# Kernel optimization log

Measured on AMD Instinct MI355X. Metric: run time of the kernel, lower is better.

The kernel has to match this reference:

```python
import jax, jax.numpy as jnp
import numpy as np

H = 4
C = 140
N0, E0 = 20000, 320000
N1, E1 = 5000, 80000
N2, E2 = 20000 // 16, 20000
N2, E2 = 1250, 20000
NSAME = 10  # conv02,11,12,21,22,14,15,16,04,05 (all 140->140)


def _seg_mean(v, idx, n):
    s = jax.ops.segment_sum(v, idx, num_segments=n)
    cnt = jax.ops.segment_sum(jnp.ones((idx.shape[0],), v.dtype), idx, num_segments=n)
    return s / jnp.maximum(cnt, 1.0)[:, None]


def _feast_conv(x, ei, W, u, c, b, n):
    # PyG FeaStConv, mean aggregation, no self loops.
    src, dst = ei[0], ei[1]
    xj = x[src]               # (E, Cin) neighbor (source) features
    xi = x[dst]               # (E, Cin) center (target) features
    q = jax.nn.softmax((xj - xi) @ u + c, axis=-1)            # (E, H)
    m = (xj @ W).reshape(xj.shape[0], H, -1)                  # (E, H, Cout)
    msg = jnp.einsum('eh,ehc->ec', q, m)                      # (E, Cout)
    return _seg_mean(msg, dst, n) + b


def _ln(h, g, be):
    mu = h.mean(-1, keepdims=True)
    v = ((h - mu) ** 2).mean(-1, keepdims=True)
    return (h - mu) * jax.lax.rsqrt(v + 1e-5) * g + be


def _block(x, ei, n, W, u, c, b, g=None, be=None, sW=None, sb=None, relu=True):
    h = _feast_conv(x, ei, W, u, c, b, n)
    if g is not None:
        h = _ln(h, g, be)
    skip = x if sW is None else x @ sW + sb
    h = h + skip
    if relu:
        h = jax.nn.relu(h)
    return h


def setup_inputs() -> dict:
    key = jax.random.key(0)
    ks = iter(jax.random.split(key, 80))

    def nrm(shape, s=0.05):
        return jax.random.normal(next(ks), shape, jnp.float32) * s

    inp = {}
    inp['x'] = jax.random.normal(next(ks), (N0, 4), jnp.float32)
    inp['e0'] = jax.random.randint(next(ks), (2, E0), 0, N0)
    inp['e1'] = jax.random.randint(next(ks), (2, E1), 0, N1)
    inp['e2'] = jax.random.randint(next(ks), (2, E2), 0, N2)
    inp['cl1'] = jax.random.randint(next(ks), (N0,), 0, N1)
    inp['cl2'] = jax.random.randint(next(ks), (N1,), 0, N2)
    inp['n0'], inp['n1'], inp['n2'] = N0, N1, N2
    # conv01: 4 -> 140 (linear skip)
    inp['W01'] = nrm((4, H * C)); inp['u01'] = nrm((4, H)); inp['c01'] = nrm((H,))
    inp['b01'] = nrm((C,)); inp['sW01'] = nrm((4, C)); inp['sb01'] = nrm((C,))
    inp['g01'] = jnp.ones((C,)); inp['be01'] = jnp.zeros((C,))
    # 10 stacked 140->140 blocks (identity skip)
    inp['Ws'] = nrm((NSAME, C, H * C)); inp['us'] = nrm((NSAME, C, H))
    inp['cs'] = nrm((NSAME, H)); inp['bs'] = nrm((NSAME, C))
    inp['gs'] = jnp.ones((NSAME, C)); inp['bes'] = jnp.zeros((NSAME, C))
    # 2 concat blocks: 280 -> 140 (conv13, conv03), linear skip
    inp['Wc'] = nrm((2, 2 * C, H * C)); inp['uc'] = nrm((2, 2 * C, H))
    inp['cc'] = nrm((2, H)); inp['bc'] = nrm((2, C))
    inp['sWc'] = nrm((2, 2 * C, C)); inp['sbc'] = nrm((2, C))
    inp['gc'] = jnp.ones((2, C)); inp['bec'] = jnp.zeros((2, C))
    # conv06: 140 -> 1, no LN, no relu, linear skip
    inp['Wo'] = nrm((C, H * 1)); inp['uo'] = nrm((C, H)); inp['co'] = nrm((H,))
    inp['bo'] = nrm((1,)); inp['sWo'] = nrm((C, 1)); inp['sbo'] = nrm((1,))
    return inp


def reference(x, W01, u01, c01, b01, sW01, sb01, g01, be01,
              Ws, us, cs, bs, gs, bes,
              Wc, uc, cc, bc, sWc, sbc, gc, bec,
              Wo, uo, co, bo, sWo, sbo,
              e0, e1, e2, cl1, cl2, n0, n1, n2):
    def same(h, i, ei, n):
        return _block(h, ei, n, Ws[i], us[i], cs[i], bs[i], gs[i], bes[i])

    def catblk(h, i, ei, n):
        return _block(h, ei, n, Wc[i], uc[i], cc[i], bc[i], gc[i], bec[i], sWc[i], sbc[i])

    h = _block(x, e0, n0, W01, u01, c01, b01, g01, be01, sW01, sb01)  # conv01
    h = same(h, 0, e0, n0)                                            # conv02
    copy0 = h
    h1 = _seg_mean(h, cl1, n1)                                        # pool1
    h1 = same(h1, 1, e1, n1)                                          # conv11
    h1 = same(h1, 2, e1, n1)                                          # conv12
    copy1 = h1
    h2 = _seg_mean(h1, cl2, n2)                                       # pool2
    h2 = same(h2, 3, e2, n2)                                          # conv21
    h2 = same(h2, 4, e2, n2)                                          # conv22
    h1 = h2[cl2]                                                      # unpool2
    h1 = jnp.concatenate((h1, copy1), axis=1)
    h1 = catblk(h1, 0, e1, n1)                                        # conv13
    h1 = same(h1, 5, e1, n1)                                          # conv14
    h1 = same(h1, 6, e1, n1)                                          # conv15
    h1 = same(h1, 7, e1, n1)                                          # conv16
    h = h1[cl1]                                                       # unpool1
    h = jnp.concatenate((h, copy0), axis=1)
    h = catblk(h, 1, e0, n0)                                          # conv03
    h = same(h, 8, e0, n0)                                            # conv04
    h = same(h, 9, e0, n0)                                            # conv05
    h = _block(h, e0, n0, Wo, uo, co, bo, None, None, sWo, sbo, relu=False)  # conv06
    return h.reshape(-1, 1)
```

## Files before the change

### kernel.cpp

```cpp
#include <hip/hip_runtime.h>
#include <math.h>

#define HH 4
#define CC 140
#define HALF 160

typedef __attribute__((ext_vector_type(8))) short short8;
typedef __attribute__((ext_vector_type(8))) _Float16 half8;
typedef __attribute__((ext_vector_type(4))) float f32x4;
typedef __attribute__((ext_vector_type(2))) _Float16 h2;
typedef unsigned short u16;

__device__ inline u16 f2h(float x) {
  union { _Float16 h; u16 u; } v; v.h = (_Float16)x; return v.u;
}
__device__ inline float h2f(u16 u) {
  union { _Float16 h; u16 u; } v; v.u = u; return (float)v.h;
}
__device__ inline h2 u2h2(unsigned u) {
  union { unsigned u; h2 h; } v; v.u = u; return v.h;
}
__device__ inline float dot2(h2 a, h2 b, float c) {
#if __has_builtin(__builtin_amdgcn_fdot2)
  return __builtin_amdgcn_fdot2(a, b, c, false);
#else
  return c + (float)a[0] * (float)b[0] + (float)a[1] * (float)b[1];
#endif
}

__global__ __launch_bounds__(256) void k_zero_i32(int* __restrict__ p, int n) {
  int i = blockIdx.x * 256 + threadIdx.x;
  if (i < n) p[i] = 0;
}
__global__ __launch_bounds__(256) void k_hist_all(
    const int* __restrict__ e0, int nE0, const int* __restrict__ e1, int nE1,
    const int* __restrict__ e2, int nE2, const int* __restrict__ cl1, int n0,
    const int* __restrict__ cl2, int n1,
    int* __restrict__ c0, int* __restrict__ c1, int* __restrict__ c2,
    int* __restrict__ c3, int* __restrict__ c4) {
  int j = blockIdx.x * 256 + threadIdx.x;
  if (j < nE0) { atomicAdd(&c0[e0[nE0 + j]], 1); return; }
  j -= nE0;
  if (j < nE1) { atomicAdd(&c1[e1[nE1 + j]], 1); return; }
  j -= nE1;
  if (j < nE2) { atomicAdd(&c2[e2[nE2 + j]], 1); return; }
  j -= nE2;
  if (j < n0) { atomicAdd(&c3[cl1[j]], 1); return; }
  j -= n0;
  if (j < n1) { atomicAdd(&c4[cl2[j]], 1); }
}
__global__ __launch_bounds__(1024) void k_exscan5(
    int* __restrict__ c0, int n0, int* __restrict__ r0,
    int* __restrict__ c1, int n1, int* __restrict__ r1,
    int* __restrict__ c2, int n2, int* __restrict__ r2,
    int* __restrict__ c3, int n3, int* __restrict__ r3,
    int* __restrict__ c4, int n4, int* __restrict__ r4) {
  int* in; int n; int* out;
  switch (blockIdx.x) {
    case 0: in = c0; n = n0; out = r0; break;
    case 1: in = c1; n = n1; out = r1; break;
    case 2: in = c2; n = n2; out = r2; break;
    case 3: in = c3; n = n3; out = r3; break;
    default: in = c4; n = n4; out = r4; break;
  }
  __shared__ int buf[1024];
  __shared__ int carry_s;
  if (threadIdx.x == 0) carry_s = 0;
  __syncthreads();
  for (int base = 0; base < n; base += 1024) {
    int i = base + (int)threadIdx.x;
    int v = (i < n) ? in[i] : 0;
    buf[threadIdx.x] = v;
    __syncthreads();
    int x = v;
    for (int off = 1; off < 1024; off <<= 1) {
      int t = (threadIdx.x >= (unsigned)off) ? buf[threadIdx.x - off] : 0;
      __syncthreads();
      x += t;
      buf[threadIdx.x] = x;
      __syncthreads();
    }
    int carry = carry_s;
    if (i < n) {
      int pref = carry + x - v;
      out[i] = pref;
      in[i] = pref;
    }
    __syncthreads();
    if (threadIdx.x == 1023) carry_s = carry + buf[1023];
    __syncthreads();
  }
  if (threadIdx.x == 0) out[n] = carry_s;
}
__global__ __launch_bounds__(256) void k_scatter_all(
    const int* __restrict__ e0, int nE0, const int* __restrict__ e1, int nE1,
    const int* __restrict__ e2, int nE2, const int* __restrict__ cl1, int n0,
    const int* __restrict__ cl2, int n1,
    int* __restrict__ c0, int* __restrict__ c1, int* __restrict__ c2,
    int* __restrict__ c3, int* __restrict__ c4,
    int* __restrict__ s0, int* __restrict__ s1, int* __restrict__ s2,
    int* __restrict__ s3, int* __restrict__ s4) {
  int j = blockIdx.x * 256 + threadIdx.x;
  if (j < nE0) { int p = atomicAdd(&c0[e0[nE0 + j]], 1); s0[p] = e0[j]; return; }
  j -= nE0;
  if (j < nE1) { int p = atomicAdd(&c1[e1[nE1 + j]], 1); s1[p] = e1[j]; return; }
  j -= nE1;
  if (j < nE2) { int p = atomicAdd(&c2[e2[nE2 + j]], 1); s2[p] = e2[j]; return; }
  j -= nE2;
  if (j < n0) { int p = atomicAdd(&c3[cl1[j]], 1); s3[p] = j; return; }
  j -= n0;
  if (j < n1) { int p = atomicAdd(&c4[cl2[j]], 1); s4[p] = j; }
}

__device__ inline void pack_one(int idx, const float* __restrict__ W,
                                const float* __restrict__ u, const float* __restrict__ sW,
                                u16* __restrict__ out, int C, int K1, int K2, int Kpad) {
  int col = idx / Kpad, kp = idx - col * Kpad;
  int ksrc = -1;
  if (kp < K1) ksrc = kp;
  else if (kp >= HALF && kp - HALF < K2) ksrc = K1 + (kp - HALF);
  float v = 0.f;
  if (ksrc >= 0) {
    if (col < 4 * C) {
      int c = col >> 2, h = col & 3;
      v = W[(size_t)ksrc * 4 * C + h * C + c];
    } else if (col < 4 * C + 4) {
      v = u[(size_t)ksrc * 4 + (col - 4 * C)];
    } else if (sW && col < 5 * C + 4) {
      v = sW[(size_t)ksrc * C + (col - 4 * C - 4)];
    }
  }
  out[idx] = f2h(v);
}
#define P01 (704 * 32)
#define PCAT (704 * 320)
#define PO (64 * 160)
#define PS (576 * 160)
__global__ __launch_bounds__(256) void k_pack_all(
    const float* __restrict__ W01, const float* __restrict__ u01, const float* __restrict__ sW01,
    const float* __restrict__ Wc, const float* __restrict__ uc, const float* __restrict__ sWc,
    const float* __restrict__ Wo, const float* __restrict__ uo, const float* __restrict__ sWo,
    const float* __restrict__ Ws, const float* __restrict__ us,
    const float* __restrict__ x,
    u16* __restrict__ Bp01, u16* __restrict__ Bpc0, u16* __restrict__ Bpc1,
    u16* __restrict__ Bpo, u16* __restrict__ Bps_all, u16* __restrict__ xb, int N0) {
  int j = blockIdx.x * 256 + threadIdx.x;
  if (j < P01) { pack_one(j, W01, u01, sW01, Bp01, CC, 4, 0, 32); return; }
  j -= P01;
  if (j < PCAT) { pack_one(j, Wc, uc, sWc, Bpc0, CC, CC, CC, 320); return; }
  j -= PCAT;
  if (j < PCAT) {
    pack_one(j, Wc + (size_t)2 * CC * HH * CC, uc + (size_t)2 * CC * HH,
             sWc + (size_t)2 * CC * CC, Bpc1, CC, CC, CC, 320);
    return;
  }
  j -= PCAT;
  if (j < PO) { pack_one(j, Wo, uo, sWo, Bpo, 1, CC, 0, 160); return; }
  j -= PO;
  if (j < 10 * PS) {
    int layer = j / PS, r = j - layer * PS;
    pack_one(r, Ws + (size_t)layer * CC * 4 * CC, us + (size_t)layer * CC * 4, nullptr,
             Bps_all + (size_t)layer * PS, CC, CC, 0, 160);
    return;
  }
  j -= 10 * PS;
  if (j < N0 * 32) {
    int i = j >> 5, c = j & 31;
    xb[j] = f2h(c < 4 ? x[(size_t)i * 4 + c] : 0.f);
  }
}

__global__ __launch_bounds__(256) void k_gemm_mfma(
    const u16* __restrict__ A1, const u16* __restrict__ A2,
    const int* __restrict__ amap, const u16* __restrict__ Bp,
    u16* __restrict__ Gy, float* __restrict__ Gl, float* __restrict__ Gs,
    int yEnd, int Cs, int N, int Kpad, int lda1) {
  __shared__ __align__(16) u16 As[128 * 32];
  __shared__ __align__(16) u16 Bs[64 * 32];
  const int tid = threadIdx.x;
  const int row0 = blockIdx.y * 128, col0 = blockIdx.x * 64;
  const int w = tid >> 6, lane = tid & 63;
  const int wm = w >> 1, wn = w & 1;
  const int arow = lane & 15, chunk = lane >> 4;
  const int swz = chunk ^ (arow & 3);
  f32x4 acc[4][2];
#pragma unroll
  for (int i = 0; i < 4; ++i)
#pragma unroll
    for (int j = 0; j < 2; ++j) acc[i][j] = (f32x4){0.f, 0.f, 0.f, 0.f};
  const int sar = tid >> 1;
  const int sak = (tid & 1) * 16;
  const int sbc = tid >> 2;
  const int sbk = (tid & 3) * 8;
  for (int k0 = 0; k0 < Kpad; k0 += 32) {
    {
      int gr = row0 + sar;
      short8 v0 = {0, 0, 0, 0, 0, 0, 0, 0}, v1 = v0;
      if (gr < N) {
        int kp0 = k0 + sak;
        const u16* b_;
        int rr, kk, ld;
        if (A2 && kp0 >= HALF) {
          b_ = A2; rr = gr; kk = kp0 - HALF; ld = HALF;
        } else {
          b_ = A1; rr = amap ? amap[gr] : gr; kk = kp0; ld = lda1;
        }
        const u16* p = b_ + (size_t)rr * ld + kk;
        v0 = *(const short8*)(p);
        v1 = *(const short8*)(p + 8);
      }
      int c0 = sak >> 3, sw = sar & 3;
      *(short8*)(As + sar * 32 + ((c0 ^ sw) << 3)) = v0;
      *(short8*)(As + sar * 32 + (((c0 + 1) ^ sw) << 3)) = v1;
    }
    {
      int gc = col0 + sbc;
      short8 v = *(const short8*)(Bp + (size_t)gc * Kpad + k0 + sbk);
      int c = sbk >> 3, sw = sbc & 3;
      *(short8*)(Bs + sbc * 32 + ((c ^ sw) << 3)) = v;
    }
    __syncthreads();
    half8 bf[2], af[4];
#pragma unroll
    for (int ni = 0; ni < 2; ++ni) {
      int col = wn * 32 + ni * 16 + arow;
      bf[ni] = *(const half8*)(Bs + col * 32 + (swz << 3));
    }
#pragma unroll
    for (int mi = 0; mi < 4; ++mi) {
      int r = wm * 64 + mi * 16 + arow;
      af[mi] = *(const half8*)(As + r * 32 + (swz << 3));
    }
#pragma unroll
    for (int mi = 0; mi < 4; ++mi)
#pragma unroll
      for (int ni = 0; ni < 2; ++ni)
        acc[mi][ni] = __builtin_amdgcn_mfma_f32_16x16x32_f16(af[mi], bf[ni], acc[mi][ni], 0, 0, 0);
    __syncthreads();
  }
  const int crow = (lane >> 4) * 4, ccol = lane & 15;
#pragma unroll
  for (int mi = 0; mi < 4; ++mi) {
    int gr0 = row0 + wm * 64 + mi * 16 + crow;
#pragma unroll
    for (int ni = 0; ni < 2; ++ni) {
      int gc = col0 + wn * 32 + ni * 16 + ccol;
#pragma unroll
      for (int j = 0; j < 4; ++j) {
        int gr = gr0 + j;
        if (gr >= N) continue;
        float v = acc[mi][ni][j];
        if (gc < yEnd) Gy[(size_t)gr * yEnd + gc] = f2h(v);
        else if (gc < yEnd + 4) Gl[(size_t)gr * 4 + (gc - yEnd)] = v;
        else if (gc < yEnd + 4 + Cs) Gs[(size_t)gr * Cs + (gc - yEnd - 4)] = v;
      }
    }
  }
}

__global__ __launch_bounds__(256) void k_agg(
    const u16* __restrict__ Gy, const float* __restrict__ Gl,
    const float* __restrict__ cv, const float* __restrict__ bias,
    const float* __restrict__ g, const float* __restrict__ be,
    const u16* __restrict__ skipA,
    const float* __restrict__ Gs, const float* __restrict__ sb,
    const int* __restrict__ rp, const int* __restrict__ sl,
    u16* __restrict__ outA, int n, int relu) {
  int wid = blockIdx.x * 4 + ((int)threadIdx.x >> 6);
  int lane = threadIdx.x & 63;
  if (wid >= n) return;
  float4 la = *(const float4*)(Gl + (size_t)wid * 4);
  float d0 = cv[0] - la.x, d1 = cv[1] - la.y;
  float d2 = cv[2] - la.z, d3 = cv[3] - la.w;
  int eb = rp[wid], ee = rp[wid + 1];
  const int c0 = lane, c1 = lane + 64, c2 = lane + 128;
  const bool h2v = c2 < CC;
  float acc0 = 0.f, acc1 = 0.f, acc2 = 0.f;
  for (int base = eb; base < ee; base += 64) {
    int m = min(ee - base, 64);
    int sreg = 0;
    int q01 = 0, q23 = 0;
    if (lane < m) {
      sreg = sl[base + lane];
      float4 lg = *(const float4*)(Gl + (size_t)sreg * 4);
      float t0 = lg.x + d0, t1 = lg.y + d1, t2 = lg.z + d2, t3 = lg.w + d3;
      float mx = fmaxf(fmaxf(t0, t1), fmaxf(t2, t3));
      float q0 = __expf(t0 - mx), q1 = __expf(t1 - mx);
      float q2 = __expf(t2 - mx), q3 = __expf(t3 - mx);
      float qi = 1.f / (q0 + q1 + q2 + q3);
      q01 = (int)((unsigned)f2h(q0 * qi) | ((unsigned)f2h(q1 * qi) << 16));
      q23 = (int)((unsigned)f2h(q2 * qi) | ((unsigned)f2h(q3 * qi) << 16));
    }
    for (int jb = 0; jb < m; jb += 8) {
      uint2 Y0[8], Y1[8], Y2[8];
      unsigned P01v[8], P23v[8];
#pragma unroll
      for (int t = 0; t < 8; ++t) {
        int j = jb + t;
        int s = __shfl(sreg, j);
        unsigned p01 = (unsigned)__shfl(q01, j);
        unsigned p23 = (unsigned)__shfl(q23, j);
        bool v = (j < m);
        P01v[t] = v ? p01 : 0u;
        P23v[t] = v ? p23 : 0u;
        if (v) {
          const u16* gy = Gy + (size_t)s * 560;
          Y0[t] = *(const uint2*)(gy + (c0 << 2));
          Y1[t] = *(const uint2*)(gy + (c1 << 2));
          Y2[t] = h2v ? *(const uint2*)(gy + (c2 << 2)) : make_uint2(0u, 0u);
        } else {
          Y0[t] = make_uint2(0u, 0u);
          Y1[t] = make_uint2(0u, 0u);
          Y2[t] = make_uint2(0u, 0u);
        }
      }
#pragma unroll
      for (int t = 0; t < 8; ++t) {
        h2 p01 = u2h2(P01v[t]), p23 = u2h2(P23v[t]);
        acc0 = dot2(u2h2(Y0[t].x), p01, acc0);
        acc0 = dot2(u2h2(Y0[t].y), p23, acc0);
        acc1 = dot2(u2h2(Y1[t].x), p01, acc1);
        acc1 = dot2(u2h2(Y1[t].y), p23, acc1);
        acc2 = dot2(u2h2(Y2[t].x), p01, acc2);
        acc2 = dot2(u2h2(Y2[t].y), p23, acc2);
      }
    }
  }
  int cnt = ee - eb;
  float inv = 1.f / (float)(cnt > 1 ? cnt : 1);
  float v0 = acc0 * inv + bias[c0];
  float v1 = acc1 * inv + bias[c1];
  float v2 = h2v ? acc2 * inv + bias[c2] : 0.f;
  if (g) {
    float s1 = v0 + v1 + v2;
    float s2 = v0 * v0 + v1 * v1 + v2 * v2;
#pragma unroll
    for (int off = 32; off > 0; off >>= 1) {
      s1 += __shfl_xor(s1, off);
      s2 += __shfl_xor(s2, off);
    }
    float mu = s1 * (1.0f / CC);
    float var = s2 * (1.0f / CC) - mu * mu;
    float r = rsqrtf(var + 1e-5f);
    v0 = (v0 - mu) * r * g[c0] + be[c0];
    v1 = (v1 - mu) * r * g[c1] + be[c1];
    if (h2v) v2 = (v2 - mu) * r * g[c2] + be[c2];
  }
  if (skipA) {
    const u16* sk = skipA + (size_t)wid * HALF;
    v0 += h2f(sk[c0]);
    v1 += h2f(sk[c1]);
    if (h2v) v2 += h2f(sk[c2]);
  } else {
    const float* gsr = Gs + (size_t)wid * CC;
    v0 += gsr[c0] + sb[c0];
    v1 += gsr[c1] + sb[c1];
    if (h2v) v2 += gsr[c2] + sb[c2];
  }
  if (relu) {
    v0 = fmaxf(v0, 0.f); v1 = fmaxf(v1, 0.f); v2 = fmaxf(v2, 0.f);
  }
  u16* oa = outA + (size_t)wid * HALF;
  oa[c0] = f2h(v0);
  oa[c1] = f2h(v1);
  if (h2v) oa[c2] = f2h(v2);
  else if (c2 < HALF) oa[c2] = 0;
}

__global__ __launch_bounds__(256) void k_out(
    const u16* __restrict__ Gy, const float* __restrict__ Gl,
    const float* __restrict__ cv, const float* __restrict__ bo,
    const float* __restrict__ Gs, const float* __restrict__ sbo,
    const int* __restrict__ rp, const int* __restrict__ sl,
    float* __restrict__ out, int n) {
  int wid = blockIdx.x * 4 + ((int)threadIdx.x >> 6);
  int lane = threadIdx.x & 63;
  if (wid >= n) return;
  float4 la = *(const float4*)(Gl + (size_t)wid * 4);
  float d0 = cv[0] - la.x, d1 = cv[1] - la.y;
  float d2 = cv[2] - la.z, d3 = cv[3] - la.w;
  int eb = rp[wid], ee = rp[wid + 1];
  float part = 0.f;
  for (int e = eb + lane; e < ee; e += 64) {
    int s = sl[e];
    float4 lg = *(const float4*)(Gl + (size_t)s * 4);
    float t0 = lg.x + d0, t1 = lg.y + d1, t2 = lg.z + d2, t3 = lg.w + d3;
    float m = fmaxf(fmaxf(t0, t1), fmaxf(t2, t3));
    float q0 = __expf(t0 - m), q1 = __expf(t1 - m), q2 = __expf(t2 - m), q3 = __expf(t3 - m);
    float qi = 1.f / (q0 + q1 + q2 + q3);
    uint2 y = *(const uint2*)(Gy + (size_t)s * 4);
    h2 y01 = u2h2(y.x), y23 = u2h2(y.y);
    part += (q0 * (float)y01[0] + q1 * (float)y01[1] +
             q2 * (float)y23[0] + q3 * (float)y23[1]) * qi;
  }
#pragma unroll
  for (int off = 32; off > 0; off >>= 1) part += __shfl_xor(part, off);
  if (lane == 0) {
    int cnt = ee - eb;
    out[wid] = part / (float)(cnt > 1 ? cnt : 1) + bo[0] + Gs[wid] + sbo[0];
  }
}

__global__ __launch_bounds__(256) void k_pool(const u16* __restrict__ inA,
                                              const int* __restrict__ rp,
                                              const int* __restrict__ sl,
                                              u16* __restrict__ outA, int nseg) {
  int wid = blockIdx.x * 4 + ((int)threadIdx.x >> 6);
  int lane = threadIdx.x & 63;
  if (wid >= nseg) return;
  int a = rp[wid], b = rp[wid + 1];
  const int c0 = lane, c1 = lane + 64, c2 = lane + 128;
  const bool h2v = c2 < CC;
  float acc0 = 0.f, acc1 = 0.f, acc2 = 0.f;
  for (int s = a; s < b; ++s) {
    size_t off = (size_t)sl[s] * HALF;
    acc0 += h2f(inA[off + c0]);
    acc1 += h2f(inA[off + c1]);
    if (h2v) acc2 += h2f(inA[off + c2]);
  }
  int cnt = b - a;
  float inv = 1.f / (float)(cnt > 1 ? cnt : 1);
  u16* oa = outA + (size_t)wid * HALF;
  oa[c0] = f2h(acc0 * inv);
  oa[c1] = f2h(acc1 * inv);
  if (h2v) oa[c2] = f2h(acc2 * inv);
  else if (c2 < HALF) oa[c2] = 0;
}

extern "C" void kernel_launch(void* const* d_in, const int* in_sizes, int n_in,
                              void* d_out, int out_size, void* d_ws, size_t ws_size,
                              hipStream_t stream) {
  (void)n_in; (void)out_size;
  const float* x    = (const float*)d_in[0];
  const int*   e0   = (const int*)d_in[1];
  const int*   e1   = (const int*)d_in[2];
  const int*   e2   = (const int*)d_in[3];
  const int*   cl1  = (const int*)d_in[4];
  const int*   cl2  = (const int*)d_in[5];
  const float* W01  = (const float*)d_in[9];
  const float* u01  = (const float*)d_in[10];
  const float* c01  = (const float*)d_in[11];
  const float* b01  = (const float*)d_in[12];
  const float* sW01 = (const float*)d_in[13];
  const float* sb01 = (const float*)d_in[14];
  const float* g01  = (const float*)d_in[15];
  const float* be01 = (const float*)d_in[16];
  const float* Ws   = (const float*)d_in[17];
  const float* us   = (const float*)d_in[18];
  const float* cs   = (const float*)d_in[19];
  const float* bs   = (const float*)d_in[20];
  const float* gs   = (const float*)d_in[21];
  const float* bes  = (const float*)d_in[22];
  const float* Wc   = (const float*)d_in[23];
  const float* uc   = (const float*)d_in[24];
  const float* cc   = (const float*)d_in[25];
  const float* bc   = (const float*)d_in[26];
  const float* sWc  = (const float*)d_in[27];
  const float* sbc  = (const float*)d_in[28];
  const float* gc   = (const float*)d_in[29];
  const float* bec  = (const float*)d_in[30];
  const float* Wo   = (const float*)d_in[31];
  const float* uo   = (const float*)d_in[32];
  const float* co   = (const float*)d_in[33];
  const float* bo   = (const float*)d_in[34];
  const float* sWo  = (const float*)d_in[35];
  const float* sbo  = (const float*)d_in[36];

  const int N0 = in_sizes[0] / 4;
  const int nE0 = in_sizes[1] / 2;
  const int nE1 = in_sizes[2] / 2;
  const int nE2 = in_sizes[3] / 2;
  const int N1 = 5000, N2 = 1250;

  float* fp = (float*)d_ws;
  auto alloc_f = [&](size_t n) { n = (n + 15) & ~(size_t)15; float* p = fp; fp += n; return p; };
  auto alloc_h = [&](size_t n) { return (u16*)alloc_f((n + 1) / 2); };
  u16*   Gy = alloc_h((size_t)N0 * 560);
  float* Gl = alloc_f((size_t)N0 * 4);
  float* Gs = alloc_f((size_t)N0 * CC);
  u16* a0A = alloc_h((size_t)N0 * HALF);
  u16* a0B = alloc_h((size_t)N0 * HALF);
  u16* a1A = alloc_h((size_t)N1 * HALF);
  u16* a1B = alloc_h((size_t)N1 * HALF);
  u16* a2A = alloc_h((size_t)N2 * HALF);
  u16* a2B = alloc_h((size_t)N2 * HALF);
  u16* xb  = alloc_h((size_t)N0 * 32);
  u16* Bp01 = alloc_h(P01);
  u16* Bpc0 = alloc_h(PCAT);
  u16* Bpc1 = alloc_h(PCAT);
  u16* Bpo  = alloc_h(PO);
  u16* Bps_all = alloc_h((size_t)10 * PS);
  u16* Bps[10];
  for (int i = 0; i < 10; ++i) Bps[i] = Bps_all + (size_t)i * PS;
  int* ipb = (int*)fp;
  auto alloc_i = [&](size_t n) { int* p = ipb; ipb += n; return p; };
  int* rp0  = alloc_i(N0 + 1);
  int* sl0  = alloc_i(nE0);
  int* rp1  = alloc_i(N1 + 1);
  int* sl1  = alloc_i(nE1);
  int* rp2  = alloc_i(N2 + 1);
  int* sl2  = alloc_i(nE2);
  int* rpc1 = alloc_i(N1 + 1);
  int* slc1 = alloc_i(N0);
  int* rpc2 = alloc_i(N2 + 1);
  int* slc2 = alloc_i(N1);
  int* cur0 = alloc_i(N0);
  int* cur1 = alloc_i(N1);
  int* cur2 = alloc_i(N2);
  int* cur3 = alloc_i(N1);
  int* cur4 = alloc_i(N2);
  const int curTot = N0 + N1 + N2 + N1 + N2;
  if ((size_t)((char*)ipb - (char*)d_ws) > ws_size) return;

  auto cdiv = [](int a, int b) { return (a + b - 1) / b; };

  k_zero_i32<<<cdiv(curTot, 256), 256, 0, stream>>>(cur0, curTot);
  {
    int tot = nE0 + nE1 + nE2 + N0 + N1;
    k_hist_all<<<cdiv(tot, 256), 256, 0, stream>>>(e0, nE0, e1, nE1, e2, nE2, cl1, N0, cl2, N1,
                                                   cur0, cur1, cur2, cur3, cur4);
    k_exscan5<<<5, 1024, 0, stream>>>(cur0, N0, rp0, cur1, N1, rp1, cur2, N2, rp2,
                                      cur3, N1, rpc1, cur4, N2, rpc2);
    k_scatter_all<<<cdiv(tot, 256), 256, 0, stream>>>(e0, nE0, e1, nE1, e2, nE2, cl1, N0, cl2, N1,
                                                      cur0, cur1, cur2, cur3, cur4,
                                                      sl0, sl1, sl2, slc1, slc2);
  }
  {
    int tot = P01 + 2 * PCAT + PO + 10 * PS + N0 * 32;
    k_pack_all<<<cdiv(tot, 256), 256, 0, stream>>>(W01, u01, sW01, Wc, uc, sWc, Wo, uo, sWo,
                                                   Ws, us, x, Bp01, Bpc0, Bpc1, Bpo,
                                                   Bps_all, xb, N0);
  }

  auto do_conv = [&](const u16* A1, const u16* A2, const int* amap, int Kpad, int lda1,
                     const u16* Bp, int Mld, bool hasSkip, int n, const int* rp, const int* sl,
                     const float* cp, const float* bp, const float* gp, const float* bep,
                     const u16* skipA, const float* sbp, u16* outA) {
    dim3 grid(Mld / 64, cdiv(n, 128));
    k_gemm_mfma<<<grid, 256, 0, stream>>>(A1, A2, amap, Bp, Gy, Gl, Gs,
                                          560, hasSkip ? CC : 0, n, Kpad, lda1);
    k_agg<<<cdiv(n, 4), 256, 0, stream>>>(Gy, Gl, cp, bp, gp, bep, skipA, Gs, sbp,
                                          rp, sl, outA, n, 1);
  };

  auto ci  = [&](int i) { return cs + (size_t)i * HH; };
  auto bi  = [&](int i) { return bs + (size_t)i * CC; };
  auto gi  = [&](int i) { return gs + (size_t)i * CC; };
  auto bei = [&](int i) { return bes + (size_t)i * CC; };

  do_conv(xb, nullptr, nullptr, 32, 32, Bp01, 704, true, N0, rp0, sl0,
          c01, b01, g01, be01, nullptr, sb01, a0A);
  do_conv(a0A, nullptr, nullptr, 160, HALF, Bps[0], 576, false, N0, rp0, sl0,
          ci(0), bi(0), gi(0), bei(0), a0A, nullptr, a0B);
  k_pool<<<cdiv(N1, 4), 256, 0, stream>>>(a0B, rpc1, slc1, a1A, N1);
  do_conv(a1A, nullptr, nullptr, 160, HALF, Bps[1], 576, false, N1, rp1, sl1,
          ci(1), bi(1), gi(1), bei(1), a1A, nullptr, a1B);
  do_conv(a1B, nullptr, nullptr, 160, HALF, Bps[2], 576, false, N1, rp1, sl1,
          ci(2), bi(2), gi(2), bei(2), a1B, nullptr, a1A);
  k_pool<<<cdiv(N2, 4), 256, 0, stream>>>(a1A, rpc2, slc2, a2A, N2);
  do_conv(a2A, nullptr, nullptr, 160, HALF, Bps[3], 576, false, N2, rp2, sl2,
          ci(3), bi(3), gi(3), bei(3), a2A, nullptr, a2B);
  do_conv(a2B, nullptr, nullptr, 160, HALF, Bps[4], 576, false, N2, rp2, sl2,
          ci(4), bi(4), gi(4), bei(4), a2B, nullptr, a2A);
  do_conv(a2A, a1A, cl2, 320, HALF, Bpc0, 704, true, N1, rp1, sl1,
          cc, bc, gc, bec, nullptr, sbc, a1B);
  do_conv(a1B, nullptr, nullptr, 160, HALF, Bps[5], 576, false, N1, rp1, sl1,
          ci(5), bi(5), gi(5), bei(5), a1B, nullptr, a1A);
  do_conv(a1A, nullptr, nullptr, 160, HALF, Bps[6], 576, false, N1, rp1, sl1,
          ci(6), bi(6), gi(6), bei(6), a1A, nullptr, a1B);
  do_conv(a1B, nullptr, nullptr, 160, HALF, Bps[7], 576, false, N1, rp1, sl1,
          ci(7), bi(7), gi(7), bei(7), a1B, nullptr, a1A);
  do_conv(a1A, a0B, cl1, 320, HALF, Bpc1, 704, true, N0, rp0, sl0,
          cc + HH, bc + CC, gc + CC, bec + CC, nullptr, sbc + CC, a0A);
  do_conv(a0A, nullptr, nullptr, 160, HALF, Bps[8], 576, false, N0, rp0, sl0,
          ci(8), bi(8), gi(8), bei(8), a0A, nullptr, a0B);
  do_conv(a0B, nullptr, nullptr, 160, HALF, Bps[9], 576, false, N0, rp0, sl0,
          ci(9), bi(9), gi(9), bei(9), a0B, nullptr, a0A);
  {
    dim3 grid(1, cdiv(N0, 128));
    k_gemm_mfma<<<grid, 256, 0, stream>>>(a0A, nullptr, nullptr, Bpo, Gy, Gl, Gs,
                                          4, 1, N0, 160, HALF);
    k_out<<<cdiv(N0, 4), 256, 0, stream>>>(Gy, Gl, co, bo, Gs, sbo, rp0, sl0, (float*)d_out, N0);
  }
}
```

Measured before the change: 670.3 us.

## Load MFMA operands directly from global memory, dropping LDS staging and barriers

The MFMA GEMM no longer stages A and B tiles through shared memory. Each lane now loads its half8 fragments straight from global memory using row pointers precomputed once per block, and the two __syncthreads per K step are gone. This removes LDS write/read traffic and barrier stalls. In exchange, tiles are reloaded redundantly across waves (wn pairs share A, wm pairs share B) and the loads become less coalesced. Out-of-range rows are clamped to N-1 instead of zero-filled, which is safe because those rows are never stored.

```diff
diff --git a/kernel.cpp b/kernel.cpp
--- a/kernel.cpp
+++ b/kernel.cpp
@@ -175,68 +175,52 @@
     const int* __restrict__ amap, const u16* __restrict__ Bp,
     u16* __restrict__ Gy, float* __restrict__ Gl, float* __restrict__ Gs,
     int yEnd, int Cs, int N, int Kpad, int lda1) {
-  __shared__ __align__(16) u16 As[128 * 32];
-  __shared__ __align__(16) u16 Bs[64 * 32];
   const int tid = threadIdx.x;
   const int row0 = blockIdx.y * 128, col0 = blockIdx.x * 64;
   const int w = tid >> 6, lane = tid & 63;
   const int wm = w >> 1, wn = w & 1;
   const int arow = lane & 15, chunk = lane >> 4;
-  const int swz = chunk ^ (arow & 3);
   f32x4 acc[4][2];
 #pragma unroll
   for (int i = 0; i < 4; ++i)
 #pragma unroll
     for (int j = 0; j < 2; ++j) acc[i][j] = (f32x4){0.f, 0.f, 0.f, 0.f};
-  const int sar = tid >> 1;
-  const int sak = (tid & 1) * 16;
-  const int sbc = tid >> 2;
-  const int sbk = (tid & 3) * 8;
+  const u16* pa1[4];
+  const u16* pa2[4];
+#pragma unroll
+  for (int mi = 0; mi < 4; ++mi) {
+    int gr = row0 + wm * 64 + mi * 16 + arow;
+    int rc = gr < N ? gr : (N - 1);
+    int rr = amap ? amap[rc] : rc;
+    pa1[mi] = A1 + (size_t)rr * lda1;
+    pa2[mi] = A2 ? A2 + (size_t)rc * HALF : nullptr;
+  }
+  const u16* pb[2];
+#pragma unroll
+  for (int ni = 0; ni < 2; ++ni) {
+    int col = col0 + wn * 32 + ni * 16 + arow;
+    pb[ni] = Bp + (size_t)col * Kpad;
+  }
+  const int co = chunk * 8;
+#pragma unroll 2
   for (int k0 = 0; k0 < Kpad; k0 += 32) {
-    {
-      int gr = row0 + sar;
-      short8 v0 = {0, 0, 0, 0, 0, 0, 0, 0}, v1 = v0;
-      if (gr < N) {
-        int kp0 = k0 + sak;
-        const u16* b_;
-        int rr, kk, ld;
-        if (A2 && kp0 >= HALF) {
-          b_ = A2; rr = gr; kk = kp0 - HALF; ld = HALF;
-        } else {
-          b_ = A1; rr = amap ? amap[gr] : gr; kk = kp0; ld = lda1;
-        }
-        const u16* p = b_ + (size_t)rr * ld + kk;
-        v0 = *(const short8*)(p);
-        v1 = *(const short8*)(p + 8);
-      }
-      int c0 = sak >> 3, sw = sar & 3;
-      *(short8*)(As + sar * 32 + ((c0 ^ sw) << 3)) = v0;
-      *(short8*)(As + sar * 32 + (((c0 + 1) ^ sw) << 3)) = v1;
-    }
-    {
-      int gc = col0 + sbc;
-      short8 v = *(const short8*)(Bp + (size_t)gc * Kpad + k0 + sbk);
-      int c = sbk >> 3, sw = sbc & 3;
-      *(short8*)(Bs + sbc * 32 + ((c ^ sw) << 3)) = v;
-    }
-    __syncthreads();
-    half8 bf[2], af[4];
+    half8 af[4], bf[2];
+    const bool useA2 = (A2 != nullptr) && (k0 >= HALF);
+    const int ka = useA2 ? (k0 - HALF) : k0;
+#pragma unroll
+    for (int mi = 0; mi < 4; ++mi) {
+      const u16* p = (useA2 ? pa2[mi] : pa1[mi]) + ka + co;
+      af[mi] = *(const half8*)(p);
+    }
 #pragma unroll
     for (int ni = 0; ni < 2; ++ni) {
-      int col = wn * 32 + ni * 16 + arow;
-      bf[ni] = *(const half8*)(Bs + col * 32 + (swz << 3));
-    }
-#pragma unroll
-    for (int mi = 0; mi < 4; ++mi) {
-      int r = wm * 64 + mi * 16 + arow;
-      af[mi] = *(const half8*)(As + r * 32 + (swz << 3));
+      bf[ni] = *(const half8*)(pb[ni] + k0 + co);
     }
 #pragma unroll
     for (int mi = 0; mi < 4; ++mi)
 #pragma unroll
       for (int ni = 0; ni < 2; ++ni)
         acc[mi][ni] = __builtin_amdgcn_mfma_f32_16x16x32_f16(af[mi], bf[ni], acc[mi][ni], 0, 0, 0);
-    __syncthreads();
   }
   const int crow = (lane >> 4) * 4, ccol = lane & 15;
 #pragma unroll
```

Result: slower. 698.5 us (+4.2%).
